# Kernel tuning notes

Hardware: AMD Instinct MI355X
Metric: run time of the kernel (lower is better)

Reference implementation:

```python
import jax, jax.numpy as jnp
import numpy as np

GAMMA = 2.0
EPS = 1e-6

B, C = 4096, 32000


def setup_inputs() -> dict:
    key = jax.random.key(0)
    k1, k2 = jax.random.split(key)
    pred = jax.random.normal(k1, (B, C), dtype=jnp.float32)
    target = jax.random.randint(k2, (B,), 0, C, dtype=jnp.int64)
    return {"pred": pred, "target": target}


def reference(pred, target):
    # pred: [B, C] logits, target: [B] int class labels
    b, c = pred.shape
    beta = (b - 1) / b
    logp = jax.nn.log_softmax(pred, axis=1)                      # [B, C]
    # Faithful to original: entropy_b = target_b * sum_c (1-p)^gamma * logp
    # (the torch code multiplies by the scalar class index b_target)
    focal = jnp.sum(jnp.power(1.0 - jnp.exp(logp), GAMMA) * logp, axis=1)  # [B]
    ent = target.astype(pred.dtype) * focal                     # [B]
    # class-balanced aggregation: bucket per class label
    counts = jax.ops.segment_sum(jnp.ones((b,), pred.dtype), target, num_segments=c)  # n_c
    cls_sum = jax.ops.segment_sum(ent, target, num_segments=c)  # sum of entropies per class
    w = (1.0 - beta) / (1.0 - jnp.power(jnp.asarray(beta, pred.dtype), counts) + EPS)
    # classes absent from batch have cls_sum == 0 exactly, so they contribute 0
    return (-1.0 / b) * jnp.sum(w * cls_sum)
```

## Files before the change

kernel.cpp:

```cpp
#include <hip/hip_runtime.h>
#include <math.h>

#define NROWS 4096
#define NCLS  32000
#define VEC_PER_ROW (NCLS / 4)
#define BLK 512
#define NV  16
#define TAIL (VEC_PER_ROW - (NV - 1) * BLK)
#define EPSF 1e-6f
#define LN2  0.69314718055994530942f
#define L2E  1.44269504088896340736f

#define LNBETA (-2.4417042724800387e-4f)
#define WNUM 2.44140625e-4f

__device__ __forceinline__ float max4(float4 v) {
    return fmaxf(fmaxf(v.x, v.y), fmaxf(v.z, v.w));
}
__device__ __forceinline__ float sum4(float4 v) {
    return (v.x + v.y) + (v.z + v.w);
}

__global__ __launch_bounds__(BLK, 4) void focal_kernel(const float* __restrict__ pred,
                                                       const int* __restrict__ target,
                                                       float* __restrict__ out)
{
    const int row = blockIdx.x;
    const int tid = threadIdx.x;
    const float4* rp = reinterpret_cast<const float4*>(pred) + (size_t)row * VEC_PER_ROW;

    float4 x[NV];
#pragma unroll
    for (int i = 0; i < NV - 1; ++i) x[i] = rp[tid + i * BLK];
    const bool lv = tid < TAIL;
    if (lv) x[NV - 1] = rp[tid + (NV - 1) * BLK];
    else    x[NV - 1] = make_float4(-1e30f, -1e30f, -1e30f, -1e30f);

    const int t_row = target[row];
    const int4* tg = reinterpret_cast<const int4*>(target);
    int4 ta = tg[tid];
    int4 tb = tg[tid + BLK];
    int cnt = (ta.x == t_row) + (ta.y == t_row) + (ta.z == t_row) + (ta.w == t_row)
            + (tb.x == t_row) + (tb.y == t_row) + (tb.z == t_row) + (tb.w == t_row);

    float m = -1e30f, s1 = 0.0f;
#pragma unroll
    for (int i = 0; i < NV - 1; ++i) { m = fmaxf(m, max4(x[i])); s1 += sum4(x[i]); }
    m = fmaxf(m, max4(x[NV - 1]));
    if (lv) s1 += sum4(x[NV - 1]);

    __shared__ float sm[8], ss[8];
    __shared__ int   sc[8];
#pragma unroll
    for (int off = 32; off > 0; off >>= 1) {
        m   = fmaxf(m, __shfl_xor(m, off));
        s1  += __shfl_xor(s1, off);
        cnt += __shfl_xor(cnt, off);
    }
    const int wid  = tid >> 6;
    const int lane = tid & 63;
    if (lane == 0) { sm[wid] = m; ss[wid] = s1; sc[wid] = cnt; }
    __syncthreads();
    if (tid < 64) {
        float mm = (tid < 8) ? sm[tid] : -1e30f;
        float s  = (tid < 8) ? ss[tid] : 0.0f;
        int   cc = (tid < 8) ? sc[tid] : 0;
#pragma unroll
        for (int off = 4; off > 0; off >>= 1) {
            mm = fmaxf(mm, __shfl_xor(mm, off));
            s += __shfl_xor(s, off);
            cc += __shfl_xor(cc, off);
        }
        if (tid == 0) { sm[0] = mm; ss[0] = s; sc[0] = cc; }
    }
    __syncthreads();
    const float M  = sm[0];
    const float S1 = ss[0];

    float Z = 0.f, A = 0.f, Z2 = 0.f, A2 = 0.f;
#pragma unroll
    for (int i = 0; i < NV; ++i) {
        float vals[4] = {x[i].x, x[i].y, x[i].z, x[i].w};
#pragma unroll
        for (int j = 0; j < 4; ++j) {
            float t = vals[j] - M;
            float e = exp2f(t * L2E);
            Z += e;
            A = fmaf(e, t, A);
            float e2 = e * e;
            Z2 += e2;
            A2 = fmaf(e2, t, A2);
        }
    }

    __shared__ float r0[8], r1[8], r2[8], r3[8];
#pragma unroll
    for (int off = 32; off > 0; off >>= 1) {
        Z  += __shfl_xor(Z,  off);
        A  += __shfl_xor(A,  off);
        Z2 += __shfl_xor(Z2, off);
        A2 += __shfl_xor(A2, off);
    }
    if (lane == 0) { r0[wid] = Z; r1[wid] = A; r2[wid] = Z2; r3[wid] = A2; }
    __syncthreads();
    if (tid < 64) {
        float a = (tid < 8) ? r0[tid] : 0.f;
        float b = (tid < 8) ? r1[tid] : 0.f;
        float c = (tid < 8) ? r2[tid] : 0.f;
        float d = (tid < 8) ? r3[tid] : 0.f;
#pragma unroll
        for (int off = 4; off > 0; off >>= 1) {
            a += __shfl_xor(a, off);
            b += __shfl_xor(b, off);
            c += __shfl_xor(c, off);
            d += __shfl_xor(d, off);
        }
        if (tid == 0) {
            float lnZ  = log2f(a) * LN2;
            float invZ = 1.0f / a;
            float T = S1 - (float)NCLS * M;
            float focal = (T - (float)NCLS * lnZ)
                        - 2.0f * (b * invZ - lnZ)
                        + (d - lnZ * c) * (invZ * invZ);

            int n = sc[0];
            float u = (float)n * LNBETA;
            float denom;
            if (u > -0.25f) {
                denom = -(u * (1.f + u * (0.5f + u * (0.16666667f + u * 0.041666667f))));
            } else {
                denom = 1.f - __expf(u);
            }
            float w = WNUM / (denom + EPSF);
            atomicAdd(out, w * (float)t_row * focal * (-1.0f / (float)NROWS));
        }
    }
}

extern "C" void kernel_launch(void* const* d_in, const int* in_sizes, int n_in,
                              void* d_out, int out_size, void* d_ws, size_t ws_size,
                              hipStream_t stream)
{
    const float* pred  = (const float*)d_in[0];
    const int* target  = (const int*)d_in[1];
    float* out         = (float*)d_out;

    hipMemsetAsync(out, 0, sizeof(float), stream);
    focal_kernel<<<NROWS, BLK, 0, stream>>>(pred, target, out);
}
```

Baseline: 104.2 us.

## Split class-count weighting into separate finalize kernel and drop memset

```diff
diff --git a/kernel.cpp b/kernel.cpp
--- a/kernel.cpp
+++ b/kernel.cpp
@@ -14,6 +14,8 @@
 #define LNBETA (-2.4417042724800387e-4f)
 #define WNUM 2.44140625e-4f
 
+#define ROWS_PER_FBLK 16
+
 __device__ __forceinline__ float max4(float4 v) {
     return fmaxf(fmaxf(v.x, v.y), fmaxf(v.z, v.w));
 }
@@ -22,11 +24,12 @@
 }
 
 __global__ __launch_bounds__(BLK, 4) void focal_kernel(const float* __restrict__ pred,
-                                                       const int* __restrict__ target,
+                                                       float* __restrict__ focal_out,
                                                        float* __restrict__ out)
 {
     const int row = blockIdx.x;
     const int tid = threadIdx.x;
+    if (row == 0 && tid == 0) out[0] = 0.0f;
     const float4* rp = reinterpret_cast<const float4*>(pred) + (size_t)row * VEC_PER_ROW;
 
     float4 x[NV];
@@ -36,13 +39,6 @@
     if (lv) x[NV - 1] = rp[tid + (NV - 1) * BLK];
     else    x[NV - 1] = make_float4(-1e30f, -1e30f, -1e30f, -1e30f);
 
-    const int t_row = target[row];
-    const int4* tg = reinterpret_cast<const int4*>(target);
-    int4 ta = tg[tid];
-    int4 tb = tg[tid + BLK];
-    int cnt = (ta.x == t_row) + (ta.y == t_row) + (ta.z == t_row) + (ta.w == t_row)
-            + (tb.x == t_row) + (tb.y == t_row) + (tb.z == t_row) + (tb.w == t_row);
-
     float m = -1e30f, s1 = 0.0f;
 #pragma unroll
     for (int i = 0; i < NV - 1; ++i) { m = fmaxf(m, max4(x[i])); s1 += sum4(x[i]); }
@@ -50,28 +46,24 @@
     if (lv) s1 += sum4(x[NV - 1]);
 
     __shared__ float sm[8], ss[8];
-    __shared__ int   sc[8];
 #pragma unroll
     for (int off = 32; off > 0; off >>= 1) {
-        m   = fmaxf(m, __shfl_xor(m, off));
-        s1  += __shfl_xor(s1, off);
-        cnt += __shfl_xor(cnt, off);
+        m  = fmaxf(m, __shfl_xor(m, off));
+        s1 += __shfl_xor(s1, off);
     }
     const int wid  = tid >> 6;
     const int lane = tid & 63;
-    if (lane == 0) { sm[wid] = m; ss[wid] = s1; sc[wid] = cnt; }
+    if (lane == 0) { sm[wid] = m; ss[wid] = s1; }
     __syncthreads();
     if (tid < 64) {
         float mm = (tid < 8) ? sm[tid] : -1e30f;
         float s  = (tid < 8) ? ss[tid] : 0.0f;
-        int   cc = (tid < 8) ? sc[tid] : 0;
 #pragma unroll
         for (int off = 4; off > 0; off >>= 1) {
             mm = fmaxf(mm, __shfl_xor(mm, off));
             s += __shfl_xor(s, off);
-            cc += __shfl_xor(cc, off);
         }
-        if (tid == 0) { sm[0] = mm; ss[0] = s; sc[0] = cc; }
+        if (tid == 0) { sm[0] = mm; ss[0] = s; }
     }
     __syncthreads();
     const float M  = sm[0];
@@ -122,18 +114,49 @@
             float focal = (T - (float)NCLS * lnZ)
                         - 2.0f * (b * invZ - lnZ)
                         + (d - lnZ * c) * (invZ * invZ);
+            focal_out[row] = focal;
+        }
+    }
+}
 
-            int n = sc[0];
-            float u = (float)n * LNBETA;
-            float denom;
-            if (u > -0.25f) {
-                denom = -(u * (1.f + u * (0.5f + u * (0.16666667f + u * 0.041666667f))));
-            } else {
-                denom = 1.f - __expf(u);
-            }
-            float w = WNUM / (denom + EPSF);
-            atomicAdd(out, w * (float)t_row * focal * (-1.0f / (float)NROWS));
+__global__ __launch_bounds__(1024) void finalize_kernel(const int* __restrict__ target,
+                                                        const float* __restrict__ focal,
+                                                        float* __restrict__ out)
+{
+    const int tid  = threadIdx.x;
+    const int wid  = tid >> 6;
+    const int lane = tid & 63;
+    const int row  = blockIdx.x * ROWS_PER_FBLK + wid;
+
+    const int t_row = target[row];
+    const int4* tg = reinterpret_cast<const int4*>(target);
+    int cnt = 0;
+#pragma unroll
+    for (int k = 0; k < NROWS / 4 / 64; ++k) {
+        int4 v = tg[lane + k * 64];
+        cnt += (v.x == t_row) + (v.y == t_row) + (v.z == t_row) + (v.w == t_row);
+    }
+#pragma unroll
+    for (int off = 32; off > 0; off >>= 1) cnt += __shfl_xor(cnt, off);
+
+    __shared__ float part[ROWS_PER_FBLK];
+    if (lane == 0) {
+        float u = (float)cnt * LNBETA;
+        float denom;
+        if (u > -0.25f) {
+            denom = -(u * (1.f + u * (0.5f + u * (0.16666667f + u * 0.041666667f))));
+        } else {
+            denom = 1.f - __expf(u);
         }
+        float w = WNUM / (denom + EPSF);
+        part[wid] = w * (float)t_row * focal[row] * (-1.0f / (float)NROWS);
+    }
+    __syncthreads();
+    if (tid == 0) {
+        float s = 0.f;
+#pragma unroll
+        for (int i = 0; i < ROWS_PER_FBLK; ++i) s += part[i];
+        atomicAdd(out, s);
     }
 }
 
@@ -145,6 +168,8 @@
     const int* target  = (const int*)d_in[1];
     float* out         = (float*)d_out;
 
-    hipMemsetAsync(out, 0, sizeof(float), stream);
-    focal_kernel<<<NROWS, BLK, 0, stream>>>(pred, target, out);
+    float* focal = (float*)d_ws;
+
+    focal_kernel<<<NROWS, BLK, 0, stream>>>(pred, focal, out);
+    finalize_kernel<<<NROWS / ROWS_PER_FBLK, 1024, 0, stream>>>(target, focal, out);
 }
```

Measured after the change: 101.6 us. -2.4%, faster.
